# Kernel optimization log

Measured on AMD Instinct MI355X. Metric: run time of the kernel, lower is better.

Reference implementation:

```python
import jax, jax.numpy as jnp
import numpy as np

B, S, T, I, H = 256, 128, 64, 63, 1024


def setup_inputs() -> dict:
    key = jax.random.key(0)
    ks = jax.random.split(key, 12)
    sc = 1.0 / np.sqrt(H)

    def rn(k, shape, scale=1.0):
        return jax.random.normal(k, shape, dtype=jnp.float32) * scale

    return dict(
        encoder_inputs=rn(ks[0], (B, S, I)),
        decoder_inputs=rn(ks[1], (B, T, I)),
        # encoder GRU params (PyTorch layout: [3H, in], gate order r,z,n)
        enc_Wih=rn(ks[2], (3 * H, I), sc), enc_Whh=rn(ks[3], (3 * H, H), sc),
        enc_bih=rn(ks[4], (3 * H,), sc), enc_bhh=rn(ks[5], (3 * H,), sc),
        # decoder GRUCell params (input dim = I, see notes)
        dec_Wih=rn(ks[6], (3 * H, I), sc), dec_Whh=rn(ks[7], (3 * H, H), sc),
        dec_bih=rn(ks[8], (3 * H,), sc), dec_bhh=rn(ks[9], (3 * H,), sc),
        # projector Linear(H -> I)
        proj_W=rn(ks[10], (I, H), sc), proj_b=rn(ks[11], (I,), sc),
    )


def _gru_gates(gi, gh, h):
    # gi = W_ih x + b_ih, gh = W_hh h + b_hh; PyTorch gate order (r, z, n)
    i_r, i_z, i_n = jnp.split(gi, 3, axis=-1)
    h_r, h_z, h_n = jnp.split(gh, 3, axis=-1)
    r = jax.nn.sigmoid(i_r + h_r)
    z = jax.nn.sigmoid(i_z + h_z)
    n = jnp.tanh(i_n + r * h_n)
    return (1.0 - z) * n + z * h


def reference(encoder_inputs, decoder_inputs, enc_Wih, enc_Whh, enc_bih,
              enc_bhh, dec_Wih, dec_Whh, dec_bih, dec_bhh, proj_W, proj_b):
    hid = enc_Whh.shape[1]
    b = encoder_inputs.shape[0]
    # ---- encoder GRU (batch_first), input-side gates precomputed as one GEMM
    gi_all = jnp.einsum('bsi,gi->bsg', encoder_inputs, enc_Wih) + enc_bih  # (B,S,3H)

    def step(h, gi):
        gh = h @ enc_Whh.T + enc_bhh
        return _gru_gates(gi, gh, h), None

    h0 = jnp.zeros((b, hid), encoder_inputs.dtype)
    enc_h, _ = jax.lax.scan(step, h0, jnp.swapaxes(gi_all, 0, 1))  # (B,H) final hidden

    # ---- decoder: per the source, every timestep feeds the SAME encoder
    # hidden state into the GRUCell (state is not carried), so all timesteps
    # are independent and can be computed as batched GEMMs over (B,T).
    gi_dec = jnp.einsum('bti,gi->btg', decoder_inputs, dec_Wih) + dec_bih   # (B,T,3H)
    gh_dec = (enc_h @ dec_Whh.T + dec_bhh)[:, None, :]                       # (B,1,3H)
    next_states = _gru_gates(gi_dec, gh_dec, enc_h[:, None, :])              # (B,T,H)

    # dropout p=0.0 (identity); projector Linear
    outputs = jnp.einsum('bth,oh->bto', next_states, proj_W) + proj_b       # (B,T,I)
    return outputs
```

## Files before the change

### kernel.cpp

```cpp
#include <hip/hip_runtime.h>


typedef unsigned short u16;
typedef unsigned int   u32;
typedef __attribute__((ext_vector_type(8))) short s8v;
typedef __attribute__((ext_vector_type(4))) float f4v;
typedef __attribute__((ext_vector_type(4))) int  i4v;

__device__ __forceinline__ float b2f(u16 u) {
    return __uint_as_float(((u32)u) << 16);
}
__device__ __forceinline__ u16 f2b(float f) {
    u32 x = __float_as_uint(f);
    u32 r = x + 0x7fffu + ((x >> 16) & 1u);
    return (u16)(r >> 16);
}
__device__ __forceinline__ float sigf(float x) {
    return 1.0f / (1.0f + __expf(-x));
}
__device__ __forceinline__ f4v mfma16(s8v a, s8v b, f4v c) {
    return __builtin_amdgcn_mfma_f32_16x16x32_bf16(a, b, c, 0, 0, 0);
}

__global__ void zero_ws(i4v* __restrict__ p, int n) {
    int i = blockIdx.x * blockDim.x + threadIdx.x;
    if (i < n) { i4v z = {0, 0, 0, 0}; p[i] = z; }
}

__global__ void conv_split(const float* __restrict__ s, u16* __restrict__ hi,
                           u16* __restrict__ lo, int n) {
    int i = blockIdx.x * blockDim.x + threadIdx.x;
    int st = gridDim.x * blockDim.x;
    for (; i < n; i += st) {
        float v = s[i];
        u16 h = f2b(v);
        hi[i] = h;
        lo[i] = f2b(v - b2f(h));
    }
}

__global__ void conv_wih_split_pad(const float* __restrict__ s,
                                   u16* __restrict__ hi, u16* __restrict__ lo) {
    int idx = blockIdx.x * blockDim.x + threadIdx.x;
    int row = idx >> 6, col = idx & 63;
    float v = (col < 63) ? s[(size_t)row * 63 + col] : 0.f;
    u16 h = f2b(v);
    hi[idx] = h;
    lo[idx] = f2b(v - b2f(h));
}

__global__ void conv_pw_split_pad(const float* __restrict__ s,
                                  u16* __restrict__ hi, u16* __restrict__ lo) {
    int idx = blockIdx.x * blockDim.x + threadIdx.x;
    float v = (idx < 63 * 1024) ? s[idx] : 0.f;
    u16 h = f2b(v);
    hi[idx] = h;
    lo[idx] = f2b(v - b2f(h));
}

template<int ROT>
__global__ __launch_bounds__(512, 1) void enc_persist(
    const u16* __restrict__ WhhH, const u16* __restrict__ WhhL,
    const u16* __restrict__ WihH, const u16* __restrict__ WihL,
    const float* __restrict__ bih, const float* __restrict__ bhh,
    const float* __restrict__ xenc,
    u16* __restrict__ hbuf, int* __restrict__ ep)
{
    __shared__ u16 BH[48 * 1032];
    __shared__ u16 BLs[2][48 * 136];
    __shared__ u16 WisH[48 * 72];
    __shared__ u16 WisL[48 * 72];
    __shared__ f4v red[4][3][64];

    if (ROT) {
        __builtin_amdgcn_fence(__ATOMIC_ACQUIRE, "agent");
    }

    const int tid  = threadIdx.x;
    const int lane = tid & 63;
    const int wave = tid >> 6;
    const int g    = wave >> 2;
    const int wv   = wave & 3;
    const int gtid = tid & 255;
    const int lrow = lane & 15;
    const int lk8  = lane >> 4;
    const int bid = blockIdx.x;
    const int y   = bid >> 3;
    const int mt  = y & 3;
    const int jt  = (bid & 7) * 8 + (y >> 2);
    const int m0 = mt * 64;
    const int j0 = jt * 16;

    int* grpCtr   = ep + mt * 16;
    int* mySlot   = ep + (mt * 64 + jt) * 16;
    int* laneSlot = ep + (mt * 64 + lane) * 16;

    #pragma unroll
    for (int i = 0; i < 12; ++i) {
        int u = i * 512 + tid;
        int row = u >> 7, p = u & 127;
        int grow = (row >> 4) * 1024 + j0 + (row & 15);
        *(i4v*)&BH[row * 1032 + p * 8] = *(const i4v*)(WhhH + (size_t)grow * 1024 + p * 8);
    }
    if (tid < 192) {
        int wr = tid >> 2, qq = tid & 3;
        int grow = (wr >> 4) * 1024 + j0 + (wr & 15);
        const u16* wpH = WihH + (size_t)grow * 64 + qq * 16;
        const u16* wpL = WihL + (size_t)grow * 64 + qq * 16;
        *(i4v*)&WisH[wr * 72 + qq * 16]     = *(const i4v*)wpH;
        *(i4v*)&WisH[wr * 72 + qq * 16 + 8] = *(const i4v*)(wpH + 8);
        *(i4v*)&WisL[wr * 72 + qq * 16]     = *(const i4v*)wpL;
        *(i4v*)&WisL[wr * 72 + qq * 16 + 8] = *(const i4v*)(wpL + 8);
    }

    const int jcol = j0 + lrow;
    const float bhr = bhh[jcol], bhz = bhh[1024 + jcol], bhn = bhh[2048 + jcol];
    const float bir = bih[jcol], biz = bih[1024 + jcol], bin = bih[2048 + jcol];

    int blrow[3], blp[3], blgrow[3];
    #pragma unroll
    for (int i = 0; i < 3; ++i) {
        int u = i * 256 + gtid;
        blrow[i] = u >> 4;
        blp[i]   = u & 15;
        blgrow[i] = (blrow[i] >> 4) * 1024 + j0 + (blrow[i] & 15);
    }

    const size_t arow = (size_t)(m0 + wv * 16 + lrow) * 1024 + lk8 * 8;
    const int kbase = g * 512;
    const float* xrow = xenc + (size_t)(m0 + wv * 16 + lrow) * 8064;

    float hprev[4] = {0.f, 0.f, 0.f, 0.f};

    i4v stgL[3];
    #pragma unroll
    for (int i = 0; i < 3; ++i)
        stgL[i] = *(const i4v*)(WhhL + (size_t)blgrow[i] * 1024 + kbase + blp[i] * 8);
    float xf[16];
    if (g == 0) {
        #pragma unroll
        for (int ks = 0; ks < 2; ++ks)
            #pragma unroll
            for (int j = 0; j < 8; ++j) {
                int col = ks * 32 + lk8 * 8 + j;
                xf[ks * 8 + j] = (col < 63) ? xrow[col] : 0.f;
            }
    }

    __syncthreads();

    for (int s = 0; s < 128; ++s) {
        const u16 *hinH, *hinL; u16 *houtH, *houtL;
        if (ROT) {
            hinH  = hbuf + (size_t)s * 524288;        hinL  = hinH + 262144;
            houtH = hbuf + (size_t)(s + 1) * 524288;  houtL = houtH + 262144;
        } else if (s & 1) {
            hinH = hbuf + 524288; hinL = hbuf + 786432;
            houtH = hbuf;         houtL = hbuf + 262144;
        } else {
            hinH = hbuf;          hinL = hbuf + 262144;
            houtH = hbuf + 524288; houtL = hbuf + 786432;
        }

        #pragma unroll
        for (int i = 0; i < 3; ++i)
            *(i4v*)&BLs[g][blrow[i] * 136 + blp[i] * 8] = stgL[i];
        __syncthreads();

        f4v acc_r  = {0.f, 0.f, 0.f, 0.f};
        f4v acc_z  = {0.f, 0.f, 0.f, 0.f};
        f4v acc_gn = {0.f, 0.f, 0.f, 0.f};
        f4v acc_hn = {0.f, 0.f, 0.f, 0.f};

        if (g == 0) {
            #pragma unroll
            for (int ks = 0; ks < 2; ++ks) {
                union { u16 a[8]; s8v v; } xh, xl;
                #pragma unroll
                for (int j = 0; j < 8; ++j) {
                    float v = xf[ks * 8 + j];
                    u16 hh = f2b(v);
                    xh.a[j] = hh;
                    xl.a[j] = f2b(v - b2f(hh));
                }
                int ao = ks * 32 + lk8 * 8;
                s8v brh = *(const s8v*)&WisH[(lrow) * 72 + ao];
                s8v brl = *(const s8v*)&WisL[(lrow) * 72 + ao];
                s8v bzh = *(const s8v*)&WisH[(16 + lrow) * 72 + ao];
                s8v bzl = *(const s8v*)&WisL[(16 + lrow) * 72 + ao];
                s8v bnh = *(const s8v*)&WisH[(32 + lrow) * 72 + ao];
                s8v bnl = *(const s8v*)&WisL[(32 + lrow) * 72 + ao];
                acc_r  = mfma16(xh.v, brh, acc_r);
                acc_r  = mfma16(xh.v, brl, acc_r);
                acc_r  = mfma16(xl.v, brh, acc_r);
                acc_z  = mfma16(xh.v, bzh, acc_z);
                acc_z  = mfma16(xh.v, bzl, acc_z);
                acc_z  = mfma16(xl.v, bzh, acc_z);
                acc_gn = mfma16(xh.v, bnh, acc_gn);
                acc_gn = mfma16(xh.v, bnl, acc_gn);
                acc_gn = mfma16(xl.v, bnh, acc_gn);
            }
        }

        const u16* hp = hinH + arow;
        const u16* lp = hinL + arow;

        for (int c = 0; c < 4; ++c) {
            if (c < 3) {
                #pragma unroll
                for (int i = 0; i < 3; ++i)
                    stgL[i] = *(const i4v*)(WhhL + (size_t)blgrow[i] * 1024 +
                                            kbase + (c + 1) * 128 + blp[i] * 8);
            }
            #pragma unroll
            for (int ks = 0; ks < 4; ++ks) {
                int kk = kbase + c * 128 + ks * 32;
                int bh = kk + lk8 * 8;
                int bl = ks * 32 + lk8 * 8;
                s8v ahi = *(const s8v*)(hp + kk);
                s8v alo = *(const s8v*)(lp + kk);
                s8v brh = *(const s8v*)&BH[(lrow) * 1032 + bh];
                s8v brl = *(const s8v*)&BLs[g][(lrow) * 136 + bl];
                s8v bzh = *(const s8v*)&BH[(16 + lrow) * 1032 + bh];
                s8v bzl = *(const s8v*)&BLs[g][(16 + lrow) * 136 + bl];
                s8v bnh = *(const s8v*)&BH[(32 + lrow) * 1032 + bh];
                s8v bnl = *(const s8v*)&BLs[g][(32 + lrow) * 136 + bl];
                acc_r  = mfma16(ahi, brh, acc_r);
                acc_r  = mfma16(ahi, brl, acc_r);
                acc_r  = mfma16(alo, brh, acc_r);
                acc_z  = mfma16(ahi, bzh, acc_z);
                acc_z  = mfma16(ahi, bzl, acc_z);
                acc_z  = mfma16(alo, bzh, acc_z);
                acc_hn = mfma16(ahi, bnh, acc_hn);
                acc_hn = mfma16(ahi, bnl, acc_hn);
                acc_hn = mfma16(alo, bnh, acc_hn);
            }
            __syncthreads();
            if (c < 3) {
                #pragma unroll
                for (int i = 0; i < 3; ++i)
                    *(i4v*)&BLs[g][blrow[i] * 136 + blp[i] * 8] = stgL[i];
                __syncthreads();
            }
        }

        if (g == 1) {
            red[wv][0][lane] = acc_r;
            red[wv][1][lane] = acc_z;
            red[wv][2][lane] = acc_hn;
        }
        __syncthreads();
        if (g == 0) {
            f4v r1 = red[wv][0][lane];
            f4v z1 = red[wv][1][lane];
            f4v n1 = red[wv][2][lane];
            #pragma unroll
            for (int reg = 0; reg < 4; ++reg) {
                int brow = m0 + wv * 16 + lk8 * 4 + reg;
                float rr = sigf(acc_r[reg] + r1[reg] + bir + bhr);
                float zz = sigf(acc_z[reg] + z1[reg] + biz + bhz);
                float nn = tanhf(acc_gn[reg] + bin + rr * (acc_hn[reg] + n1[reg] + bhn));
                float h = (1.f - zz) * nn + zz * hprev[reg];
                u16 hh = f2b(h);
                u16 ll = f2b(h - b2f(hh));
                hprev[reg] = b2f(hh) + b2f(ll);
                size_t off = (size_t)brow * 1024 + jcol;
                if (ROT) {
                    __hip_atomic_store(&houtH[off], hh, __ATOMIC_RELAXED,
                                       __HIP_MEMORY_SCOPE_SYSTEM);
                    __hip_atomic_store(&houtL[off], ll, __ATOMIC_RELAXED,
                                       __HIP_MEMORY_SCOPE_SYSTEM);
                } else {
                    houtH[off] = hh;
                    houtL[off] = ll;
                }
            }
        }

        __syncthreads();
        if (ROT) {
            if (tid == 0)
                __hip_atomic_fetch_add(grpCtr, 1, __ATOMIC_RELAXED,
                                       __HIP_MEMORY_SCOPE_SYSTEM);
        } else if (tid == 0) {
            __builtin_amdgcn_fence(__ATOMIC_RELEASE, "agent");
            __hip_atomic_store(mySlot, s + 1, __ATOMIC_RELAXED,
                               __HIP_MEMORY_SCOPE_AGENT);
        }
        #pragma unroll
        for (int i = 0; i < 3; ++i)
            stgL[i] = *(const i4v*)(WhhL + (size_t)blgrow[i] * 1024 + kbase + blp[i] * 8);
        if (g == 0) {
            int sn = (s < 127) ? s + 1 : 127;
            const float* xr = xrow + sn * 63;
            #pragma unroll
            for (int ks = 0; ks < 2; ++ks)
                #pragma unroll
                for (int j = 0; j < 8; ++j) {
                    int col = ks * 32 + lk8 * 8 + j;
                    xf[ks * 8 + j] = (col < 63) ? xr[col] : 0.f;
                }
        }
        if (ROT) {
            if (wave == 0 && lane == 0) {
                int tgt = (s + 1) << 6;
                while (__hip_atomic_load(grpCtr, __ATOMIC_RELAXED,
                                         __HIP_MEMORY_SCOPE_SYSTEM) < tgt)
                    __builtin_amdgcn_s_sleep(1);
            }
        } else if (wave == 0) {
            for (;;) {
                int v = __hip_atomic_load(laneSlot, __ATOMIC_RELAXED,
                                          __HIP_MEMORY_SCOPE_AGENT);
                if (__all(v >= s + 1)) break;
                __builtin_amdgcn_s_sleep(2);
            }
            __builtin_amdgcn_fence(__ATOMIC_ACQUIRE, "agent");
        }
        __syncthreads();
    }
}

__global__ __launch_bounds__(256, 1) void gru_gemm1(
    const u16* __restrict__ WhhH, const u16* __restrict__ WhhL,
    const float* __restrict__ bhh,
    const u16* __restrict__ hin_hi, const u16* __restrict__ hin_lo,
    float* __restrict__ gh_out)
{
    __shared__ u16 WbH[48 * 264];
    __shared__ u16 WbL[48 * 264];

    const int tid  = threadIdx.x;
    const int lane = tid & 63;
    const int wave = tid >> 6;
    const int lrow = lane & 15;
    const int lk8  = lane >> 4;
    const int mt = blockIdx.x & 3;
    const int jt = blockIdx.x >> 2;
    const int m0 = mt * 64;
    const int j0 = jt * 16;

    f4v acc_r  = {0.f, 0.f, 0.f, 0.f};
    f4v acc_z  = {0.f, 0.f, 0.f, 0.f};
    f4v acc_hn = {0.f, 0.f, 0.f, 0.f};

    i4v stgH[6], stgL[6];
    #pragma unroll
    for (int i = 0; i < 6; ++i) {
        int c16 = i * 256 + tid;
        int row = c16 >> 5, p16 = c16 & 31;
        int grow = (row >> 4) * 1024 + j0 + (row & 15);
        size_t off = (size_t)grow * 1024 + p16 * 8;
        stgH[i] = *(const i4v*)(WhhH + off);
        stgL[i] = *(const i4v*)(WhhL + off);
    }
    #pragma unroll
    for (int i = 0; i < 6; ++i) {
        int c16 = i * 256 + tid;
        int row = c16 >> 5, p16 = c16 & 31;
        *(i4v*)&WbH[row * 264 + p16 * 8] = stgH[i];
        *(i4v*)&WbL[row * 264 + p16 * 8] = stgL[i];
    }
    __syncthreads();

    const size_t arow = (size_t)(m0 + wave * 16 + lrow) * 1024 + lk8 * 8;
    const u16* hp = hin_hi + arow;
    const u16* lp = hin_lo + arow;

    for (int c = 0; c < 4; ++c) {
        if (c < 3) {
            #pragma unroll
            for (int i = 0; i < 6; ++i) {
                int c16 = i * 256 + tid;
                int row = c16 >> 5, p16 = c16 & 31;
                int grow = (row >> 4) * 1024 + j0 + (row & 15);
                size_t off = (size_t)grow * 1024 + (c + 1) * 256 + p16 * 8;
                stgH[i] = *(const i4v*)(WhhH + off);
                stgL[i] = *(const i4v*)(WhhL + off);
            }
        }
        #pragma unroll
        for (int ks = 0; ks < 8; ++ks) {
            int kk = c * 256 + ks * 32;
            int bo = ks * 32 + lk8 * 8;
            s8v ahi = *(const s8v*)(hp + kk);
            s8v alo = *(const s8v*)(lp + kk);
            s8v brh = *(const s8v*)&WbH[(lrow) * 264 + bo];
            s8v brl = *(const s8v*)&WbL[(lrow) * 264 + bo];
            s8v bzh = *(const s8v*)&WbH[(16 + lrow) * 264 + bo];
            s8v bzl = *(const s8v*)&WbL[(16 + lrow) * 264 + bo];
            s8v bnh = *(const s8v*)&WbH[(32 + lrow) * 264 + bo];
            s8v bnl = *(const s8v*)&WbL[(32 + lrow) * 264 + bo];
            acc_r  = mfma16(ahi, brh, acc_r);
            acc_r  = mfma16(ahi, brl, acc_r);
            acc_r  = mfma16(alo, brh, acc_r);
            acc_z  = mfma16(ahi, bzh, acc_z);
            acc_z  = mfma16(ahi, bzl, acc_z);
            acc_z  = mfma16(alo, bzh, acc_z);
            acc_hn = mfma16(ahi, bnh, acc_hn);
            acc_hn = mfma16(ahi, bnl, acc_hn);
            acc_hn = mfma16(alo, bnh, acc_hn);
        }
        __syncthreads();
        if (c < 3) {
            #pragma unroll
            for (int i = 0; i < 6; ++i) {
                int c16 = i * 256 + tid;
                int row = c16 >> 5, p16 = c16 & 31;
                *(i4v*)&WbH[row * 264 + p16 * 8] = stgH[i];
                *(i4v*)&WbL[row * 264 + p16 * 8] = stgL[i];
            }
            __syncthreads();
        }
    }

    const int jcol = j0 + lrow;
    const float bhr = bhh[jcol];
    const float bhz = bhh[1024 + jcol];
    const float bhn = bhh[2048 + jcol];
    #pragma unroll
    for (int reg = 0; reg < 4; ++reg) {
        int brow = m0 + wave * 16 + lk8 * 4 + reg;
        gh_out[(size_t)brow * 3072 + jcol]        = acc_r[reg] + bhr;
        gh_out[(size_t)brow * 3072 + 1024 + jcol] = acc_z[reg] + bhz;
        gh_out[(size_t)brow * 3072 + 2048 + jcol] = acc_hn[reg] + bhn;
    }
}

__global__ __launch_bounds__(256, 1) void dec_fused(
    const u16* __restrict__ WihH, const u16* __restrict__ WihL,
    const float* __restrict__ bih,
    const float* __restrict__ xdec,
    const u16* __restrict__ ehi, const u16* __restrict__ elo,
    const float* __restrict__ gh,
    const u16* __restrict__ pWH, const u16* __restrict__ pWL,
    const float* __restrict__ pb,
    float* __restrict__ out)
{
    __shared__ u16 XdH[64 * 72];
    __shared__ u16 XdL[64 * 72];
    __shared__ u16 WiH_[192 * 72];
    __shared__ u16 WiL_[192 * 72];
    __shared__ u16 nsH[64 * 72];
    __shared__ u16 nsL[64 * 72];

    const int tid  = threadIdx.x;
    const int lane = tid & 63;
    const int wave = tid >> 6;
    const int lrow = lane & 15;
    const int lk8  = lane >> 4;
    const int b    = blockIdx.x;

    {
        int row = tid >> 2, q = tid & 3;
        const float* xr = xdec + (size_t)(b * 64 + row) * 63;
        #pragma unroll
        for (int ii = 0; ii < 16; ++ii) {
            int col = q * 16 + ii;
            float v = (col < 63) ? xr[col] : 0.f;
            u16 hh = f2b(v);
            XdH[row * 72 + col] = hh;
            XdL[row * 72 + col] = f2b(v - b2f(hh));
        }
    }

    f4v oacc[4];
    #pragma unroll
    for (int f = 0; f < 4; ++f) oacc[f] = f4v{0.f, 0.f, 0.f, 0.f};

    for (int j0 = 0; j0 < 1024; j0 += 64) {
        #pragma unroll
        for (int k = 0; k < 3; ++k) {
            int c = tid + k * 256;
            int r = c >> 2, qq = c & 3;
            int grow = (r >> 6) * 1024 + j0 + (r & 63);
            const u16* srcH = WihH + (size_t)grow * 64 + qq * 16;
            const u16* srcL = WihL + (size_t)grow * 64 + qq * 16;
            *(i4v*)&WiH_[r * 72 + qq * 16]     = *(const i4v*)srcH;
            *(i4v*)&WiH_[r * 72 + qq * 16 + 8] = *(const i4v*)(srcH + 8);
            *(i4v*)&WiL_[r * 72 + qq * 16]     = *(const i4v*)srcL;
            *(i4v*)&WiL_[r * 72 + qq * 16 + 8] = *(const i4v*)(srcL + 8);
        }
        __syncthreads();

        f4v ar[4], az[4], an[4];
        #pragma unroll
        for (int jf = 0; jf < 4; ++jf) {
            ar[jf] = f4v{0.f, 0.f, 0.f, 0.f};
            az[jf] = f4v{0.f, 0.f, 0.f, 0.f};
            an[jf] = f4v{0.f, 0.f, 0.f, 0.f};
        }
        #pragma unroll
        for (int ks = 0; ks < 2; ++ks) {
            int ao = ks * 32 + lk8 * 8;
            s8v ah = *(const s8v*)&XdH[(wave * 16 + lrow) * 72 + ao];
            s8v al = *(const s8v*)&XdL[(wave * 16 + lrow) * 72 + ao];
            #pragma unroll
            for (int jf = 0; jf < 4; ++jf) {
                s8v brh = *(const s8v*)&WiH_[(jf * 16 + lrow) * 72 + ao];
                s8v brl = *(const s8v*)&WiL_[(jf * 16 + lrow) * 72 + ao];
                s8v bzh = *(const s8v*)&WiH_[(64 + jf * 16 + lrow) * 72 + ao];
                s8v bzl = *(const s8v*)&WiL_[(64 + jf * 16 + lrow) * 72 + ao];
                s8v bnh = *(const s8v*)&WiH_[(128 + jf * 16 + lrow) * 72 + ao];
                s8v bnl = *(const s8v*)&WiL_[(128 + jf * 16 + lrow) * 72 + ao];
                ar[jf] = mfma16(ah, brh, ar[jf]);
                ar[jf] = mfma16(ah, brl, ar[jf]);
                ar[jf] = mfma16(al, brh, ar[jf]);
                az[jf] = mfma16(ah, bzh, az[jf]);
                az[jf] = mfma16(ah, bzl, az[jf]);
                az[jf] = mfma16(al, bzh, az[jf]);
                an[jf] = mfma16(ah, bnh, an[jf]);
                an[jf] = mfma16(ah, bnl, an[jf]);
                an[jf] = mfma16(al, bnh, an[jf]);
            }
        }

        #pragma unroll
        for (int jf = 0; jf < 4; ++jf) {
            int j = j0 + jf * 16 + lrow;
            float ghr = gh[(size_t)b * 3072 + j];
            float ghz = gh[(size_t)b * 3072 + 1024 + j];
            float ghn = gh[(size_t)b * 3072 + 2048 + j];
            float bir = bih[j];
            float biz = bih[1024 + j];
            float bin = bih[2048 + j];
            size_t eo = (size_t)b * 1024 + j;
            float he = b2f(ehi[eo]) + b2f(elo[eo]);
            #pragma unroll
            for (int reg = 0; reg < 4; ++reg) {
                float r  = sigf(ar[jf][reg] + bir + ghr);
                float z  = sigf(az[jf][reg] + biz + ghz);
                float nn = tanhf(an[jf][reg] + bin + r * ghn);
                float v  = (1.f - z) * nn + z * he;
                u16 hh = f2b(v);
                int lo_i = (wave * 16 + lk8 * 4 + reg) * 72 + jf * 16 + lrow;
                nsH[lo_i] = hh;
                nsL[lo_i] = f2b(v - b2f(hh));
            }
        }
        __syncthreads();

        #pragma unroll
        for (int ks = 0; ks < 2; ++ks) {
            int ao = ks * 32 + lk8 * 8;
            s8v ah = *(const s8v*)&nsH[(wave * 16 + lrow) * 72 + ao];
            s8v al = *(const s8v*)&nsL[(wave * 16 + lrow) * 72 + ao];
            #pragma unroll
            for (int f = 0; f < 4; ++f) {
                size_t bo = (size_t)(f * 16 + lrow) * 1024 + j0 + ks * 32 + lk8 * 8;
                s8v bh = *(const s8v*)(pWH + bo);
                s8v bl = *(const s8v*)(pWL + bo);
                oacc[f] = mfma16(ah, bh, oacc[f]);
                oacc[f] = mfma16(ah, bl, oacc[f]);
                oacc[f] = mfma16(al, bh, oacc[f]);
            }
        }
        __syncthreads();
    }

    #pragma unroll
    for (int f = 0; f < 4; ++f) {
        int o = f * 16 + lrow;
        if (o < 63) {
            float pbv = pb[o];
            #pragma unroll
            for (int reg = 0; reg < 4; ++reg) {
                int t = wave * 16 + lk8 * 4 + reg;
                out[((size_t)(b * 64 + t)) * 63 + o] = oacc[f][reg] + pbv;
            }
        }
    }
}

extern "C" void kernel_launch(void* const* d_in, const int* in_sizes, int n_in,
                              void* d_out, int out_size, void* d_ws, size_t ws_size,
                              hipStream_t stream)
{
    const float* enc_x = (const float*)d_in[0];
    const float* dec_x = (const float*)d_in[1];
    const float* eWih  = (const float*)d_in[2];
    const float* eWhh  = (const float*)d_in[3];
    const float* ebih  = (const float*)d_in[4];
    const float* ebhh  = (const float*)d_in[5];
    const float* dWih  = (const float*)d_in[6];
    const float* dWhh  = (const float*)d_in[7];
    const float* dbih  = (const float*)d_in[8];
    const float* dbhh  = (const float*)d_in[9];
    const float* pW    = (const float*)d_in[10];
    const float* pb    = (const float*)d_in[11];

    char* ws = (char*)d_ws;

    const size_t ROT_NEED = 165429248ull;
    const bool rot = (ws_size >= ROT_NEED);

    u16 *hbuf, *Hfin_hi, *Hfin_lo;
    int* ep;
    float* ghd;
    u16 *eWhhH, *eWhhL, *dWhhH, *dWhhL;
    u16 *eWihH, *eWihL, *dWihH, *dWihL;
    u16 *pWH, *pWL;

    if (rot) {
        hbuf  = (u16*)(ws);
        ep    = (int*)(ws + 135266304);
        ghd   = (float*)(ws + 135282688);
        eWhhH = (u16*)(ws + 138428416);
        eWhhL = (u16*)(ws + 144719872);
        dWhhH = (u16*)(ws + 151011328);
        dWhhL = (u16*)(ws + 157302784);
        eWihH = (u16*)(ws + 163594240);
        eWihL = (u16*)(ws + 163987456);
        dWihH = (u16*)(ws + 164380672);
        dWihL = (u16*)(ws + 164773888);
        pWH   = (u16*)(ws + 165167104);
        pWL   = (u16*)(ws + 165298176);
        Hfin_hi = hbuf + (size_t)128 * 524288;
        Hfin_lo = Hfin_hi + 262144;
    } else {
        hbuf  = (u16*)(ws);
        ep    = (int*)(ws + 2097152);
        ghd   = (float*)(ws + 3145728);
        eWhhH = (u16*)(ws + 6291456);
        eWhhL = (u16*)(ws + 12582912);
        dWhhH = (u16*)(ws + 18874368);
        dWhhL = (u16*)(ws + 25165824);
        eWihH = (u16*)(ws + 31457280);
        eWihL = (u16*)(ws + 31850496);
        dWihH = (u16*)(ws + 32243712);
        dWihL = (u16*)(ws + 32636928);
        pWH   = (u16*)(ws + 33030144);
        pWL   = (u16*)(ws + 33161216);
        Hfin_hi = hbuf;
        Hfin_lo = hbuf + 262144;
    }

    conv_split<<<dim3(4096), dim3(256), 0, stream>>>(eWhh, eWhhH, eWhhL, 3145728);
    conv_split<<<dim3(4096), dim3(256), 0, stream>>>(dWhh, dWhhH, dWhhL, 3145728);
    conv_wih_split_pad<<<dim3(768), dim3(256), 0, stream>>>(eWih, eWihH, eWihL);
    conv_wih_split_pad<<<dim3(768), dim3(256), 0, stream>>>(dWih, dWihH, dWihL);
    conv_pw_split_pad<<<dim3(256), dim3(256), 0, stream>>>(pW, pWH, pWL);

    if (rot) {
        zero_ws<<<dim3(256), dim3(256), 0, stream>>>((i4v*)hbuf, 65536);
        zero_ws<<<dim3(4), dim3(256), 0, stream>>>((i4v*)ep, 1024);
        enc_persist<1><<<dim3(256), dim3(512), 0, stream>>>(
            eWhhH, eWhhL, eWihH, eWihL, ebih, ebhh, enc_x, hbuf, ep);
    } else {
        zero_ws<<<dim3(517), dim3(256), 0, stream>>>((i4v*)ws, 132096);
        enc_persist<0><<<dim3(256), dim3(512), 0, stream>>>(
            eWhhH, eWhhL, eWihH, eWihL, ebih, ebhh, enc_x, hbuf, ep);
    }

    gru_gemm1<<<dim3(256), dim3(256), 0, stream>>>(
        dWhhH, dWhhL, dbhh, Hfin_hi, Hfin_lo, ghd);

    dec_fused<<<dim3(256), dim3(256), 0, stream>>>(
        dWihH, dWihL, dbih, dec_x, Hfin_hi, Hfin_lo, ghd, pWH, pWL, pb,
        (float*)d_out);
}
```

Measured before the change: 1.663 ms.

## Keep encoder recurrent weights in registers and use per-XCD sub-counters for sync

In the rotating-buffer path, the encoder persistent kernel is replaced by a version that holds each block's slice of W_hh (hi/lo bf16 split) in VGPRs instead of LDS. Each of the 8 waves covers a separate 128-wide K slice across all four M tiles, and the partial sums are reduced through shared memory. The single per-group atomic counter, which 64 blocks contended on, becomes 8 per-XCD sub-counters that wave 0 polls across lanes. This targets the per-step LDS traffic for weights and the atomic contention, at the cost of heavy register pressure and a larger cross-wave reduction.

Measured after the change: 1.554 ms. 6.6% less time.

```diff
diff --git a/kernel.cpp b/kernel.cpp
--- a/kernel.cpp
+++ b/kernel.cpp
@@ -58,8 +58,215 @@
     lo[idx] = f2b(v - b2f(h));
 }
 
-template<int ROT>
-__global__ __launch_bounds__(512, 1) void enc_persist(
+__global__ __launch_bounds__(512, 1) void enc_persist_reg(
+    const u16* __restrict__ WhhH, const u16* __restrict__ WhhL,
+    const u16* __restrict__ WihH, const u16* __restrict__ WihL,
+    const float* __restrict__ bih, const float* __restrict__ bhh,
+    const float* __restrict__ xenc,
+    u16* __restrict__ hbuf, int* __restrict__ ep)
+{
+    __shared__ f4v red[8][4][3][64];
+    __shared__ u16 WisH[48 * 72];
+    __shared__ u16 WisL[48 * 72];
+
+    __builtin_amdgcn_fence(__ATOMIC_ACQUIRE, "agent");
+
+    const int tid  = threadIdx.x;
+    const int lane = tid & 63;
+    const int wave = tid >> 6;
+    const int lrow = lane & 15;
+    const int lk8  = lane >> 4;
+    const int bid = blockIdx.x;
+    const int xcd = bid & 7;
+    const int y   = bid >> 3;
+    const int mt  = y & 3;
+    const int jt  = xcd * 8 + (y >> 2);
+    const int m0 = mt * 64;
+    const int j0 = jt * 16;
+
+    int* subCtr  = ep + (mt * 8 + xcd) * 16;
+    int* pollCtr = ep + (mt * 8 + (lane & 7)) * 16;
+
+    if (tid < 192) {
+        int wr = tid >> 2, qq = tid & 3;
+        int grow = (wr >> 4) * 1024 + j0 + (wr & 15);
+        const u16* wpH = WihH + (size_t)grow * 64 + qq * 16;
+        const u16* wpL = WihL + (size_t)grow * 64 + qq * 16;
+        *(i4v*)&WisH[wr * 72 + qq * 16]     = *(const i4v*)wpH;
+        *(i4v*)&WisH[wr * 72 + qq * 16 + 8] = *(const i4v*)(wpH + 8);
+        *(i4v*)&WisL[wr * 72 + qq * 16]     = *(const i4v*)wpL;
+        *(i4v*)&WisL[wr * 72 + qq * 16 + 8] = *(const i4v*)(wpL + 8);
+    }
+
+    s8v bHf[3][4], bLf[3][4];
+    const int k0 = wave * 128;
+    #pragma unroll
+    for (int gg = 0; gg < 3; ++gg)
+        #pragma unroll
+        for (int ks = 0; ks < 4; ++ks) {
+            size_t off = (size_t)(gg * 1024 + j0 + lrow) * 1024 +
+                         k0 + ks * 32 + lk8 * 8;
+            bHf[gg][ks] = *(const s8v*)(WhhH + off);
+            bLf[gg][ks] = *(const s8v*)(WhhL + off);
+        }
+
+    const int jcol = j0 + lrow;
+    const float bhr = bhh[jcol], bhz = bhh[1024 + jcol], bhn = bhh[2048 + jcol];
+    const float bir = bih[jcol], biz = bih[1024 + jcol], bin = bih[2048 + jcol];
+
+    size_t aoff[4];
+    #pragma unroll
+    for (int mtile = 0; mtile < 4; ++mtile)
+        aoff[mtile] = (size_t)(m0 + mtile * 16 + lrow) * 1024 + k0 + lk8 * 8;
+
+    const float* xrow = xenc + (size_t)(m0 + (wave & 3) * 16 + lrow) * 8064;
+    float hprev[4] = {0.f, 0.f, 0.f, 0.f};
+
+    float xf[16];
+    if (wave < 4) {
+        #pragma unroll
+        for (int ks = 0; ks < 2; ++ks)
+            #pragma unroll
+            for (int j = 0; j < 8; ++j) {
+                int col = ks * 32 + lk8 * 8 + j;
+                xf[ks * 8 + j] = (col < 63) ? xrow[col] : 0.f;
+            }
+    }
+
+    __syncthreads();
+
+    for (int s = 0; s < 128; ++s) {
+        const u16* hinH = hbuf + (size_t)s * 524288;
+        const u16* hinL = hinH + 262144;
+        u16* houtH = hbuf + (size_t)(s + 1) * 524288;
+        u16* houtL = houtH + 262144;
+
+        f4v accr[4], accz[4], acchn[4];
+        #pragma unroll
+        for (int m = 0; m < 4; ++m) {
+            accr[m]  = f4v{0.f, 0.f, 0.f, 0.f};
+            accz[m]  = f4v{0.f, 0.f, 0.f, 0.f};
+            acchn[m] = f4v{0.f, 0.f, 0.f, 0.f};
+        }
+        f4v gi_r = {0.f, 0.f, 0.f, 0.f};
+        f4v gi_z = {0.f, 0.f, 0.f, 0.f};
+        f4v gi_n = {0.f, 0.f, 0.f, 0.f};
+
+        if (wave < 4) {
+            #pragma unroll
+            for (int ks = 0; ks < 2; ++ks) {
+                union { u16 a[8]; s8v v; } xh, xl;
+                #pragma unroll
+                for (int j = 0; j < 8; ++j) {
+                    float v = xf[ks * 8 + j];
+                    u16 hh = f2b(v);
+                    xh.a[j] = hh;
+                    xl.a[j] = f2b(v - b2f(hh));
+                }
+                int ao = ks * 32 + lk8 * 8;
+                s8v brh = *(const s8v*)&WisH[(lrow) * 72 + ao];
+                s8v brl = *(const s8v*)&WisL[(lrow) * 72 + ao];
+                s8v bzh = *(const s8v*)&WisH[(16 + lrow) * 72 + ao];
+                s8v bzl = *(const s8v*)&WisL[(16 + lrow) * 72 + ao];
+                s8v bnh = *(const s8v*)&WisH[(32 + lrow) * 72 + ao];
+                s8v bnl = *(const s8v*)&WisL[(32 + lrow) * 72 + ao];
+                gi_r = mfma16(xh.v, brh, gi_r);
+                gi_r = mfma16(xh.v, brl, gi_r);
+                gi_r = mfma16(xl.v, brh, gi_r);
+                gi_z = mfma16(xh.v, bzh, gi_z);
+                gi_z = mfma16(xh.v, bzl, gi_z);
+                gi_z = mfma16(xl.v, bzh, gi_z);
+                gi_n = mfma16(xh.v, bnh, gi_n);
+                gi_n = mfma16(xh.v, bnl, gi_n);
+                gi_n = mfma16(xl.v, bnh, gi_n);
+            }
+        }
+
+        #pragma unroll
+        for (int mtile = 0; mtile < 4; ++mtile) {
+            #pragma unroll
+            for (int ks = 0; ks < 4; ++ks) {
+                s8v ahi = *(const s8v*)(hinH + aoff[mtile] + ks * 32);
+                s8v alo = *(const s8v*)(hinL + aoff[mtile] + ks * 32);
+                accr[mtile]  = mfma16(ahi, bHf[0][ks], accr[mtile]);
+                accr[mtile]  = mfma16(ahi, bLf[0][ks], accr[mtile]);
+                accr[mtile]  = mfma16(alo, bHf[0][ks], accr[mtile]);
+                accz[mtile]  = mfma16(ahi, bHf[1][ks], accz[mtile]);
+                accz[mtile]  = mfma16(ahi, bLf[1][ks], accz[mtile]);
+                accz[mtile]  = mfma16(alo, bHf[1][ks], accz[mtile]);
+                acchn[mtile] = mfma16(ahi, bHf[2][ks], acchn[mtile]);
+                acchn[mtile] = mfma16(ahi, bLf[2][ks], acchn[mtile]);
+                acchn[mtile] = mfma16(alo, bHf[2][ks], acchn[mtile]);
+            }
+        }
+
+        #pragma unroll
+        for (int m = 0; m < 4; ++m) {
+            f4v pr = accr[m], pz = accz[m];
+            if (wave == m) { pr += gi_r; pz += gi_z; }
+            red[wave][m][0][lane] = pr;
+            red[wave][m][1][lane] = pz;
+            red[wave][m][2][lane] = acchn[m];
+        }
+        __syncthreads();
+
+        if (wave < 4) {
+            f4v sr = {0.f, 0.f, 0.f, 0.f};
+            f4v sz = {0.f, 0.f, 0.f, 0.f};
+            f4v sh = {0.f, 0.f, 0.f, 0.f};
+            #pragma unroll
+            for (int w = 0; w < 8; ++w) {
+                sr += red[w][wave][0][lane];
+                sz += red[w][wave][1][lane];
+                sh += red[w][wave][2][lane];
+            }
+            #pragma unroll
+            for (int reg = 0; reg < 4; ++reg) {
+                int brow = m0 + wave * 16 + lk8 * 4 + reg;
+                float rr = sigf(sr[reg] + bir + bhr);
+                float zz = sigf(sz[reg] + biz + bhz);
+                float nn = tanhf(gi_n[reg] + bin + rr * (sh[reg] + bhn));
+                float h = (1.f - zz) * nn + zz * hprev[reg];
+                u16 hh = f2b(h);
+                u16 ll = f2b(h - b2f(hh));
+                hprev[reg] = b2f(hh) + b2f(ll);
+                size_t off = (size_t)brow * 1024 + jcol;
+                __hip_atomic_store(&houtH[off], hh, __ATOMIC_RELAXED,
+                                   __HIP_MEMORY_SCOPE_SYSTEM);
+                __hip_atomic_store(&houtL[off], ll, __ATOMIC_RELAXED,
+                                   __HIP_MEMORY_SCOPE_SYSTEM);
+            }
+        }
+
+        __syncthreads();
+        if (tid == 0)
+            __hip_atomic_fetch_add(subCtr, 1, __ATOMIC_RELAXED,
+                                   __HIP_MEMORY_SCOPE_SYSTEM);
+        if (wave < 4) {
+            int sn = (s < 127) ? s + 1 : 127;
+            const float* xr = xrow + sn * 63;
+            #pragma unroll
+            for (int ks = 0; ks < 2; ++ks)
+                #pragma unroll
+                for (int j = 0; j < 8; ++j) {
+                    int col = ks * 32 + lk8 * 8 + j;
+                    xf[ks * 8 + j] = (col < 63) ? xr[col] : 0.f;
+                }
+        }
+        if (wave == 0) {
+            int tgt = (s + 1) * 8;
+            for (;;) {
+                int v = __hip_atomic_load(pollCtr, __ATOMIC_RELAXED,
+                                          __HIP_MEMORY_SCOPE_SYSTEM);
+                if (__all(v >= tgt)) break;
+                __builtin_amdgcn_s_sleep(1);
+            }
+        }
+        __syncthreads();
+    }
+}
+
+__global__ __launch_bounds__(512, 1) void enc_persist_legacy(
     const u16* __restrict__ WhhH, const u16* __restrict__ WhhL,
     const u16* __restrict__ WihH, const u16* __restrict__ WihL,
     const float* __restrict__ bih, const float* __restrict__ bhh,
@@ -71,10 +278,6 @@
     __shared__ u16 WisH[48 * 72];
     __shared__ u16 WisL[48 * 72];
     __shared__ f4v red[4][3][64];
-
-    if (ROT) {
-        __builtin_amdgcn_fence(__ATOMIC_ACQUIRE, "agent");
-    }
 
     const int tid  = threadIdx.x;
     const int lane = tid & 63;
@@ -91,7 +294,6 @@
     const int m0 = mt * 64;
     const int j0 = jt * 16;
 
-    int* grpCtr   = ep + mt * 16;
     int* mySlot   = ep + (mt * 64 + jt) * 16;
     int* laneSlot = ep + (mt * 64 + lane) * 16;
 
@@ -151,10 +353,7 @@
 
     for (int s = 0; s < 128; ++s) {
         const u16 *hinH, *hinL; u16 *houtH, *houtL;
-        if (ROT) {
-            hinH  = hbuf + (size_t)s * 524288;        hinL  = hinH + 262144;
-            houtH = hbuf + (size_t)(s + 1) * 524288;  houtL = houtH + 262144;
-        } else if (s & 1) {
+        if (s & 1) {
             hinH = hbuf + 524288; hinL = hbuf + 786432;
             houtH = hbuf;         houtL = hbuf + 262144;
         } else {
@@ -265,24 +464,13 @@
                 u16 ll = f2b(h - b2f(hh));
                 hprev[reg] = b2f(hh) + b2f(ll);
                 size_t off = (size_t)brow * 1024 + jcol;
-                if (ROT) {
-                    __hip_atomic_store(&houtH[off], hh, __ATOMIC_RELAXED,
-                                       __HIP_MEMORY_SCOPE_SYSTEM);
-                    __hip_atomic_store(&houtL[off], ll, __ATOMIC_RELAXED,
-                                       __HIP_MEMORY_SCOPE_SYSTEM);
-                } else {
-                    houtH[off] = hh;
-                    houtL[off] = ll;
-                }
-            }
-        }
-
-        __syncthreads();
-        if (ROT) {
-            if (tid == 0)
-                __hip_atomic_fetch_add(grpCtr, 1, __ATOMIC_RELAXED,
-                                       __HIP_MEMORY_SCOPE_SYSTEM);
-        } else if (tid == 0) {
+                houtH[off] = hh;
+                houtL[off] = ll;
+            }
+        }
+
+        __syncthreads();
+        if (tid == 0) {
             __builtin_amdgcn_fence(__ATOMIC_RELEASE, "agent");
             __hip_atomic_store(mySlot, s + 1, __ATOMIC_RELAXED,
                                __HIP_MEMORY_SCOPE_AGENT);
@@ -301,14 +489,7 @@
                     xf[ks * 8 + j] = (col < 63) ? xr[col] : 0.f;
                 }
         }
-        if (ROT) {
-            if (wave == 0 && lane == 0) {
-                int tgt = (s + 1) << 6;
-                while (__hip_atomic_load(grpCtr, __ATOMIC_RELAXED,
-                                         __HIP_MEMORY_SCOPE_SYSTEM) < tgt)
-                    __builtin_amdgcn_s_sleep(1);
-            }
-        } else if (wave == 0) {
+        if (wave == 0) {
             for (;;) {
                 int v = __hip_atomic_load(laneSlot, __ATOMIC_RELAXED,
                                           __HIP_MEMORY_SCOPE_AGENT);
@@ -644,11 +825,11 @@
     if (rot) {
         zero_ws<<<dim3(256), dim3(256), 0, stream>>>((i4v*)hbuf, 65536);
         zero_ws<<<dim3(4), dim3(256), 0, stream>>>((i4v*)ep, 1024);
-        enc_persist<1><<<dim3(256), dim3(512), 0, stream>>>(
+        enc_persist_reg<<<dim3(256), dim3(512), 0, stream>>>(
             eWhhH, eWhhL, eWihH, eWihL, ebih, ebhh, enc_x, hbuf, ep);
     } else {
         zero_ws<<<dim3(517), dim3(256), 0, stream>>>((i4v*)ws, 132096);
-        enc_persist<0><<<dim3(256), dim3(512), 0, stream>>>(
+        enc_persist_legacy<<<dim3(256), dim3(512), 0, stream>>>(
             eWhhH, eWhhL, eWihH, eWihL, ebih, ebhh, enc_x, hbuf, ep);
     }
 
```
